# Kernel optimization log

Measured on AMD Instinct MI355X. Metric: run time of the kernel, lower is better.

## Reference

```python
import jax, jax.numpy as jnp
import numpy as np

B, T, NIN = 128, 256, 16
H1 = H2 = 512
NACT = 4
SLOPE = 25.0  # snntorch FastSigmoid default slope

@jax.custom_vjp
def spike(x):
    return (x > 0).astype(x.dtype)

def _spike_fwd(x):
    return (x > 0).astype(x.dtype), x

def _spike_bwd(x, g):
    # FastSigmoid surrogate: d/dx = 1 / (slope*|x| + 1)^2
    return (g / (SLOPE * jnp.abs(x) + 1.0) ** 2,)

spike.defvjp(_spike_fwd, _spike_bwd)

def setup_inputs() -> dict:
    key = jax.random.key(0)
    ks = jax.random.split(key, 12)
    def lin(k, fan_in, shape):
        lim = 1.0 / np.sqrt(fan_in)
        return jax.random.uniform(k, shape, jnp.float32, -lim, lim)
    return {
        "batch": jax.random.uniform(ks[0], (B, T, NIN), jnp.float32, 0.0, 2.5),
        "W1": lin(ks[1], NIN, (H1, NIN)), "b1": lin(ks[2], NIN, (H1,)),
        "beta1": jax.random.uniform(ks[3], (H1,), jnp.float32),
        "thr1": jax.random.uniform(ks[4], (H1,), jnp.float32),
        "W2": lin(ks[5], H1, (H2, H1)), "b2": lin(ks[6], H1, (H2,)),
        "beta2": jax.random.uniform(ks[7], (H2,), jnp.float32),
        "thr2": jax.random.uniform(ks[8], (H2,), jnp.float32),
        "Wa": lin(ks[9], H2, (NACT, H2)), "ba": lin(ks[10], H2, (NACT,)),
        "beta_act": jnp.float32(0.95),
        "inp_min": jnp.float32(0.0),
        "inp_max": jnp.float32(2.5),
    }

def _lif_subtract(cur, mem, beta, thr):
    # snntorch Leaky: reset from PRE-update membrane, detached; subtract reset
    reset = jax.lax.stop_gradient((mem - thr > 0).astype(mem.dtype))
    mem = jnp.clip(beta, 0.0, 1.0) * mem + cur - reset * thr
    return spike(mem - thr), mem

def reference(batch, W1, b1, beta1, thr1, W2, b2, beta2, thr2, Wa, ba, beta_act, inp_min, inp_max):
    Bb = batch.shape[0]
    x_seq = jnp.swapaxes(batch, 0, 1)  # [T, B, NIN]
    mem1 = jnp.zeros((Bb, W1.shape[0]), batch.dtype)
    mem2 = jnp.zeros((Bb, W2.shape[0]), batch.dtype)
    mem_a = jnp.zeros((Bb, Wa.shape[0]), batch.dtype)

    def step(carry, x):
        mem1, mem2, mem_a = carry
        x = (x - inp_min) / (inp_max - inp_min)
        spk1, mem1 = _lif_subtract(x @ W1.T + b1, mem1, beta1, thr1)
        spk2, mem2 = _lif_subtract(spk1 @ W2.T + b2, mem2, beta2, thr2)
        act = spk2 @ Wa.T + ba
        # action_lif: reset_mechanism='none', beta=0.95 learnable
        mem_a = jnp.clip(beta_act, 0.0, 1.0) * mem_a + act
        return (mem1, mem2, mem_a), mem_a.reshape(-1)  # torch: mem_act.reshape((1,-1))

    _, vals = jax.lax.scan(step, (mem1, mem2, mem_a), x_seq)
    # torch.stack(values, dim=1) of (1, B*NACT) tensors -> (1, T, B*NACT)
    return vals[None, :, :]
```

## Files before the change

### kernel.cpp

```cpp
#include <hip/hip_runtime.h>
#include <stdint.h>

typedef __attribute__((ext_vector_type(8))) short short8;
typedef __attribute__((ext_vector_type(4))) float f32x4;

#define T_STEPS 256
#define BATCH   128

#define LDS_BARRIER() asm volatile("s_waitcnt lgkmcnt(0)\n\ts_barrier" ::: "memory")

static __device__ inline unsigned short f2bf(float f) {
    unsigned int u = __float_as_uint(f);
    unsigned int r = u + 0x7FFFu + ((u >> 16) & 1u);
    return (unsigned short)(r >> 16);
}
static __device__ inline unsigned pack_hi16(unsigned a, unsigned b) {
    return (a >> 16) | (b & 0xFFFF0000u);
}

__global__ __launch_bounds__(256) void k_prep(
    const float* __restrict__ W2, const float* __restrict__ W1,
    const float* __restrict__ b1, const float* __restrict__ thr1,
    const float* __restrict__ imin_p, const float* __restrict__ imax_p,
    const float* __restrict__ batch,
    unsigned short* __restrict__ W2hi, unsigned short* __restrict__ W2lo,
    unsigned short* __restrict__ W1rows, float* __restrict__ b1s,
    unsigned short* __restrict__ Xf)
{
    int blk = blockIdx.x, tid = threadIdx.x;
    if (blk < 256) {
        int gid = blk * 256 + tid;
        f32x4 wv = *(const f32x4*)(W2 + (size_t)gid * 4);
        unsigned short hi[4], lo[4];
#pragma unroll
        for (int e = 0; e < 4; ++e) {
            float wf = wv[e];
            unsigned short h = f2bf(wf);
            float hf = __uint_as_float(((unsigned int)h) << 16);
            hi[e] = h;
            lo[e] = f2bf(wf - hf);
        }
        uint2 ph, pl;
        ph.x = (unsigned)hi[0] | ((unsigned)hi[1] << 16);
        ph.y = (unsigned)hi[2] | ((unsigned)hi[3] << 16);
        pl.x = (unsigned)lo[0] | ((unsigned)lo[1] << 16);
        pl.y = (unsigned)lo[2] | ((unsigned)lo[3] << 16);
        *(uint2*)(W2hi + (size_t)gid * 4) = ph;
        *(uint2*)(W2lo + (size_t)gid * 4) = pl;
    } else if (blk < 258) {
        int h = (blk - 256) * 256 + tid;
        float wsc = 1.0f / thr1[h];
        unsigned short row[64];
#pragma unroll
        for (int k = 0; k < 16; ++k) {
            float wv = W1[h * 16 + k] * wsc;
            unsigned a = __float_as_uint(wv) & 0xFFFF0000u;
            float r1 = wv - __uint_as_float(a);
            unsigned m = __float_as_uint(r1) & 0xFFFF0000u;
            float r2 = r1 - __uint_as_float(m);
            unsigned l = __float_as_uint(r2) & 0xFFFF0000u;
            row[k]      = (unsigned short)(a >> 16);
            row[16 + k] = (unsigned short)(m >> 16);
            row[32 + k] = (unsigned short)(l >> 16);
            row[48 + k] = 0;
        }
        b1s[h] = b1[h] * wsc;
        uint4* dst = (uint4*)(W1rows + (size_t)h * 64);
#pragma unroll
        for (int i = 0; i < 8; ++i) dst[i] = ((uint4*)row)[i];
    } else {
        int gid   = (blk - 258) * 256 + tid;
        int lane  = gid & 63;
        int btile = (gid >> 6) & 7;
        int t     = gid >> 9;
        int q     = lane >> 4, m15 = lane & 15;
        int b     = btile * 16 + m15;
        float imin = imin_p[0];
        float isc  = 1.0f / (imax_p[0] - imin);
        const float* xp = batch + ((size_t)b * T_STEPS + t) * 16 + (q & 1) * 8;
        unsigned uh[8], um[8], ul[8];
#pragma unroll
        for (int j = 0; j < 8; ++j) {
            float xv = (xp[j] - imin) * isc;
            unsigned a = __float_as_uint(xv) & 0xFFFF0000u;
            float r1 = xv - __uint_as_float(a);
            unsigned m = __float_as_uint(r1) & 0xFFFF0000u;
            float r2 = r1 - __uint_as_float(m);
            unsigned l = __float_as_uint(r2) & 0xFFFF0000u;
            uh[j] = a; um[j] = m; ul[j] = l;
        }
        uint4 B1, B2, XL;
        B1.x = pack_hi16(uh[0], uh[1]); B1.y = pack_hi16(uh[2], uh[3]);
        B1.z = pack_hi16(uh[4], uh[5]); B1.w = pack_hi16(uh[6], uh[7]);
        B2.x = pack_hi16(um[0], um[1]); B2.y = pack_hi16(um[2], um[3]);
        B2.z = pack_hi16(um[4], um[5]); B2.w = pack_hi16(um[6], um[7]);
        XL.x = pack_hi16(ul[0], ul[1]); XL.y = pack_hi16(ul[2], ul[3]);
        XL.z = pack_hi16(ul[4], ul[5]); XL.w = pack_hi16(ul[6], ul[7]);
        uint4 B3 = (q < 2) ? XL : B1;
        uint4 B4 = (q < 2) ? XL : B2;
        unsigned short* dst = Xf + (((size_t)t * 8 + btile) * 4) * 512 + lane * 8;
        *(uint4*)(dst +    0) = B1;
        *(uint4*)(dst +  512) = B2;
        *(uint4*)(dst + 1024) = B3;
        *(uint4*)(dst + 1536) = B4;
    }
}

__global__ __launch_bounds__(1024, 4) void k_main(
    const unsigned short* __restrict__ Xf,
    const unsigned short* __restrict__ W2hi, const unsigned short* __restrict__ W2lo,
    const unsigned short* __restrict__ W1rows, const float* __restrict__ b1s,
    const float* __restrict__ beta1, const float* __restrict__ b2,
    const float* __restrict__ beta2, const float* __restrict__ thr2,
    unsigned short* __restrict__ spkbits)
{
    __shared__ unsigned short Aw[8192];
    __shared__ float Cbuf[2][4096];

    int tid  = threadIdx.x;
    int lane = tid & 63;
    int w    = tid >> 6;
    int q    = lane >> 4, m15 = lane & 15;
    int btile = blockIdx.x & 7;
    int slice = blockIdx.x >> 3;

    short8 A1[2], A2[2], A3[2];
#pragma unroll
    for (int c = 0; c < 2; ++c) {
        const unsigned short* rp = W1rows + (size_t)(w * 32 + c * 16 + m15) * 64;
        A1[c] = *(const short8*)(rp + q * 8);
        A2[c] = *(const short8*)(rp + q * 8 + (q >> 1) * 16);
        A3[c] = *(const short8*)(rp + 16 + q * 8);
    }
    int jg = slice * 16 + m15;
    short8 bhi = *(const short8*)(W2hi + (size_t)jg * 512 + w * 32 + q * 8);
    short8 blo = *(const short8*)(W2lo + (size_t)jg * 512 + w * 32 + q * 8);

    f32x4 b14[2], bet1[2];
#pragma unroll
    for (int c = 0; c < 2; ++c) {
        int h0 = w * 32 + c * 16 + q * 4;
        b14[c] = *(const f32x4*)(b1s + h0);
        f32x4 bb = *(const f32x4*)(beta1 + h0);
#pragma unroll
        for (int r = 0; r < 4; ++r) bet1[c][r] = fminf(fmaxf(bb[r], 0.0f), 1.0f);
    }
    float m1[8], spk1f[8];
#pragma unroll
    for (int i = 0; i < 8; ++i) { m1[i] = 0.0f; spk1f[i] = 0.0f; }

    float beta2r = fminf(fmaxf(beta2[jg], 0.0f), 1.0f);
    float thr2r  = thr2[jg];
    float nthr2  = -thr2r;
    float b2r    = b2[jg];
    float m2 = 0.0f, spk2f = 0.0f;

    const unsigned short* xbase = Xf + ((size_t)btile * 4) * 512 + lane * 8;
    uint4 xc[4], xn[4];
#pragma unroll
    for (int f = 0; f < 4; ++f) xc[f] = *(const uint4*)(xbase + f * 512);

    unsigned short* myAw = Aw + w * 512;
    int wr0 = (0 * 2 + (q >> 1)) * 128 + (m15 ^ (q >> 1)) * 8 + (q & 1) * 4;
    int wr1 = (1 * 2 + (q >> 1)) * 128 + (m15 ^ (q >> 1)) * 8 + (q & 1) * 4;
    int rdo = (q * 16 + (m15 ^ (q & 1))) * 8;

    auto body = [&](int ts, uint4* xcur, uint4* xnx) __attribute__((always_inline)) {
        int buf = ts & 1;
        int tn = (ts + 1 < T_STEPS) ? ts + 1 : ts;
        const unsigned short* xp = xbase + (size_t)tn * 16384;
#pragma unroll
        for (int f = 0; f < 4; ++f) xnx[f] = *(const uint4*)(xp + f * 512);

        union { uint4 u; short8 s; } Bf[4];
#pragma unroll
        for (int f = 0; f < 4; ++f) Bf[f].u = xcur[f];
        f32x4 D[2];
#pragma unroll
        for (int c = 0; c < 2; ++c) {
            D[c] = b14[c];
            D[c] = __builtin_amdgcn_mfma_f32_16x16x32_bf16(A1[c], Bf[0].s, D[c], 0, 0, 0);
            D[c] = __builtin_amdgcn_mfma_f32_16x16x32_bf16(A1[c], Bf[1].s, D[c], 0, 0, 0);
            D[c] = __builtin_amdgcn_mfma_f32_16x16x32_bf16(A2[c], Bf[2].s, D[c], 0, 0, 0);
            D[c] = __builtin_amdgcn_mfma_f32_16x16x32_bf16(A3[c], Bf[3].s, D[c], 0, 0, 0);
        }
#pragma unroll
        for (int i = 0; i < 8; ++i) {
            int c = i >> 2, r = i & 3;
            float mv = fmaf(bet1[c][r], m1[i], D[c][r]);
            mv -= spk1f[i];
            bool sp = mv > 1.0f;
            m1[i] = mv;
            spk1f[i] = sp ? 1.0f : 0.0f;
        }
        {
            uint2 pk0, pk1;
            pk0.x = pack_hi16(__float_as_uint(spk1f[0]), __float_as_uint(spk1f[1]));
            pk0.y = pack_hi16(__float_as_uint(spk1f[2]), __float_as_uint(spk1f[3]));
            pk1.x = pack_hi16(__float_as_uint(spk1f[4]), __float_as_uint(spk1f[5]));
            pk1.y = pack_hi16(__float_as_uint(spk1f[6]), __float_as_uint(spk1f[7]));
            *(uint2*)(myAw + wr0) = pk0;
            *(uint2*)(myAw + wr1) = pk1;
        }
        union { uint4 u; short8 s; } af;
        af.u = *(uint4*)(myAw + rdo);
        f32x4 C2 = { 0.f, 0.f, 0.f, 0.f };
        C2 = __builtin_amdgcn_mfma_f32_16x16x32_bf16(af.s, bhi, C2, 0, 0, 0);
        C2 = __builtin_amdgcn_mfma_f32_16x16x32_bf16(af.s, blo, C2, 0, 0, 0);
#pragma unroll
        for (int r = 0; r < 4; ++r)
            Cbuf[buf][r * 1024 + w * 64 + lane] = C2[r];
        LDS_BARRIER();
        if (w < 4) {
            float cur2 = b2r;
#pragma unroll
            for (int wp = 0; wp < 16; ++wp) cur2 += Cbuf[buf][w * 1024 + wp * 64 + lane];
            m2 = fmaf(beta2r, m2, cur2);
            m2 = fmaf(spk2f, nthr2, m2);
            bool sp2 = m2 > thr2r;
            spk2f = sp2 ? 1.0f : 0.0f;
            unsigned long long mask = __ballot(sp2);
            if (lane < 4) {
                unsigned short v = (unsigned short)(mask >> (lane * 16));
                spkbits[((size_t)ts * BATCH + btile * 16 + lane * 4 + w) * 32 + slice] = v;
            }
        }
    };

#pragma unroll 1
    for (int ts = 0; ts < T_STEPS; ts += 2) {
        body(ts, xc, xn);
        body(ts + 1, xn, xc);
    }
}

__global__ __launch_bounds__(256) void k_act(
    const unsigned short* __restrict__ spkbits,
    const float* __restrict__ Wa, const float* __restrict__ ba,
    const float* __restrict__ beta_act_p, float* __restrict__ out)
{
    __shared__ f32x4 waT[512];
    __shared__ f32x4 sc[256];
    int tid = threadIdx.x;
    int b   = blockIdx.x;

    for (int j = tid; j < 512; j += 256) {
        f32x4 v = { Wa[j], Wa[512 + j], Wa[1024 + j], Wa[1536 + j] };
        waT[j] = v;
    }
    float bact = fminf(fmaxf(beta_act_p[0], 0.0f), 1.0f);
    f32x4 acc = { ba[0], ba[1], ba[2], ba[3] };
    __syncthreads();

    const unsigned short* sp = spkbits + ((size_t)tid * BATCH + b) * 32;
    unsigned int wbuf[16];
#pragma unroll
    for (int r = 0; r < 4; ++r) {
        uint4 v = *(const uint4*)(sp + r * 8);
        wbuf[r*4+0] = v.x; wbuf[r*4+1] = v.y; wbuf[r*4+2] = v.z; wbuf[r*4+3] = v.w;
    }
    for (int s = 0; s < 32; ++s) {
        unsigned int wd = (wbuf[s >> 1] >> ((s & 1) * 16)) & 0xFFFFu;
#pragma unroll
        for (int i = 0; i < 16; ++i) {
            float sel = ((wd >> i) & 1u) ? 1.0f : 0.0f;
            f32x4 wv = waT[s * 16 + i];
            acc[0] = fmaf(sel, wv[0], acc[0]);
            acc[1] = fmaf(sel, wv[1], acc[1]);
            acc[2] = fmaf(sel, wv[2], acc[2]);
            acc[3] = fmaf(sel, wv[3], acc[3]);
        }
    }
    sc[tid] = acc;
    __syncthreads();
    float bd = bact;
    for (int d = 1; d < 256; d <<= 1) {
        f32x4 cv = sc[tid];
        f32x4 pv = { 0.f, 0.f, 0.f, 0.f };
        if (tid >= d) pv = sc[tid - d];
        __syncthreads();
        cv[0] = fmaf(bd, pv[0], cv[0]);
        cv[1] = fmaf(bd, pv[1], cv[1]);
        cv[2] = fmaf(bd, pv[2], cv[2]);
        cv[3] = fmaf(bd, pv[3], cv[3]);
        sc[tid] = cv;
        __syncthreads();
        bd *= bd;
    }
    f32x4 res = sc[tid];
    *(f32x4*)(out + (size_t)tid * 512 + b * 4) = res;
}

extern "C" void kernel_launch(void* const* d_in, const int* in_sizes, int n_in,
                              void* d_out, int out_size, void* d_ws, size_t ws_size,
                              hipStream_t stream)
{
    const float* batch    = (const float*)d_in[0];
    const float* W1       = (const float*)d_in[1];
    const float* b1       = (const float*)d_in[2];
    const float* beta1    = (const float*)d_in[3];
    const float* thr1     = (const float*)d_in[4];
    const float* W2       = (const float*)d_in[5];
    const float* b2       = (const float*)d_in[6];
    const float* beta2    = (const float*)d_in[7];
    const float* thr2     = (const float*)d_in[8];
    const float* Wa       = (const float*)d_in[9];
    const float* ba       = (const float*)d_in[10];
    const float* beta_act = (const float*)d_in[11];
    const float* inp_min  = (const float*)d_in[12];
    const float* inp_max  = (const float*)d_in[13];
    float* out            = (float*)d_out;

    char* ws = (char*)d_ws;
    unsigned short* W2hi    = (unsigned short*)ws;
    unsigned short* W2lo    = (unsigned short*)(ws + (512u << 10));
    unsigned short* W1rows  = (unsigned short*)(ws + (1u << 20));
    float*          b1s     = (float*)(ws + (1u << 20) + (64u << 10));
    unsigned short* Xf      = (unsigned short*)(ws + (2u << 20));
    unsigned short* spkbits = (unsigned short*)(ws + (10u << 20));

    hipLaunchKernelGGL(k_prep, dim3(770), dim3(256), 0, stream,
                       W2, W1, b1, thr1, inp_min, inp_max, batch,
                       W2hi, W2lo, W1rows, b1s, Xf);
    hipLaunchKernelGGL(k_main, dim3(256), dim3(1024), 0, stream,
                       Xf, W2hi, W2lo, W1rows, b1s, beta1, b2, beta2, thr2, spkbits);
    hipLaunchKernelGGL(k_act, dim3(128), dim3(256), 0, stream, spkbits, Wa, ba, beta_act, out);
}
```

Baseline: 308.7 us.

## Drop redundant x fragment MFMA and spread layer-2 reduction across all waves

The layer-1 input projection now uses three split-bf16 fragments instead of four. This removes one MFMA per tile and one global load stream per step, and shrinks the staged input buffer. The cross-wave reduction of layer-2 partial sums is re-laid out with a padded transposed LDS buffer. All 16 waves now each sum four partials and finish with shuffles, where before four waves serially summed sixteen. The change removes work from the per-step critical path, but it relies on the dropped fragment being redundant for accuracy.

```diff
diff --git a/kernel.cpp b/kernel.cpp
--- a/kernel.cpp
+++ b/kernel.cpp
@@ -97,12 +97,10 @@
         XL.x = pack_hi16(ul[0], ul[1]); XL.y = pack_hi16(ul[2], ul[3]);
         XL.z = pack_hi16(ul[4], ul[5]); XL.w = pack_hi16(ul[6], ul[7]);
         uint4 B3 = (q < 2) ? XL : B1;
-        uint4 B4 = (q < 2) ? XL : B2;
-        unsigned short* dst = Xf + (((size_t)t * 8 + btile) * 4) * 512 + lane * 8;
+        unsigned short* dst = Xf + (((size_t)t * 8 + btile) * 3) * 512 + lane * 8;
         *(uint4*)(dst +    0) = B1;
         *(uint4*)(dst +  512) = B2;
         *(uint4*)(dst + 1024) = B3;
-        *(uint4*)(dst + 1536) = B4;
     }
 }
 
@@ -115,7 +113,7 @@
     unsigned short* __restrict__ spkbits)
 {
     __shared__ unsigned short Aw[8192];
-    __shared__ float Cbuf[2][4096];
+    __shared__ float Cbuf[2][4352];
 
     int tid  = threadIdx.x;
     int lane = tid & 63;
@@ -124,13 +122,12 @@
     int btile = blockIdx.x & 7;
     int slice = blockIdx.x >> 3;
 
-    short8 A1[2], A2[2], A3[2];
+    short8 A1[2], A2[2];
 #pragma unroll
     for (int c = 0; c < 2; ++c) {
         const unsigned short* rp = W1rows + (size_t)(w * 32 + c * 16 + m15) * 64;
         A1[c] = *(const short8*)(rp + q * 8);
         A2[c] = *(const short8*)(rp + q * 8 + (q >> 1) * 16);
-        A3[c] = *(const short8*)(rp + 16 + q * 8);
     }
     int jg = slice * 16 + m15;
     short8 bhi = *(const short8*)(W2hi + (size_t)jg * 512 + w * 32 + q * 8);
@@ -155,26 +152,27 @@
     float b2r    = b2[jg];
     float m2 = 0.0f, spk2f = 0.0f;
 
-    const unsigned short* xbase = Xf + ((size_t)btile * 4) * 512 + lane * 8;
-    uint4 xc[4], xn[4];
-#pragma unroll
-    for (int f = 0; f < 4; ++f) xc[f] = *(const uint4*)(xbase + f * 512);
+    const unsigned short* xbase = Xf + ((size_t)btile * 3) * 512 + lane * 8;
+    uint4 xc[3], xn[3];
+#pragma unroll
+    for (int f = 0; f < 3; ++f) xc[f] = *(const uint4*)(xbase + f * 512);
 
     unsigned short* myAw = Aw + w * 512;
     int wr0 = (0 * 2 + (q >> 1)) * 128 + (m15 ^ (q >> 1)) * 8 + (q & 1) * 4;
     int wr1 = (1 * 2 + (q >> 1)) * 128 + (m15 ^ (q >> 1)) * 8 + (q & 1) * 4;
     int rdo = (q * 16 + (m15 ^ (q & 1))) * 8;
+    int p4  = (lane >> 4) * 4;
 
     auto body = [&](int ts, uint4* xcur, uint4* xnx) __attribute__((always_inline)) {
         int buf = ts & 1;
         int tn = (ts + 1 < T_STEPS) ? ts + 1 : ts;
-        const unsigned short* xp = xbase + (size_t)tn * 16384;
-#pragma unroll
-        for (int f = 0; f < 4; ++f) xnx[f] = *(const uint4*)(xp + f * 512);
-
-        union { uint4 u; short8 s; } Bf[4];
-#pragma unroll
-        for (int f = 0; f < 4; ++f) Bf[f].u = xcur[f];
+        const unsigned short* xp = xbase + (size_t)tn * 12288;
+#pragma unroll
+        for (int f = 0; f < 3; ++f) xnx[f] = *(const uint4*)(xp + f * 512);
+
+        union { uint4 u; short8 s; } Bf[3];
+#pragma unroll
+        for (int f = 0; f < 3; ++f) Bf[f].u = xcur[f];
         f32x4 D[2];
 #pragma unroll
         for (int c = 0; c < 2; ++c) {
@@ -182,7 +180,6 @@
             D[c] = __builtin_amdgcn_mfma_f32_16x16x32_bf16(A1[c], Bf[0].s, D[c], 0, 0, 0);
             D[c] = __builtin_amdgcn_mfma_f32_16x16x32_bf16(A1[c], Bf[1].s, D[c], 0, 0, 0);
             D[c] = __builtin_amdgcn_mfma_f32_16x16x32_bf16(A2[c], Bf[2].s, D[c], 0, 0, 0);
-            D[c] = __builtin_amdgcn_mfma_f32_16x16x32_bf16(A3[c], Bf[3].s, D[c], 0, 0, 0);
         }
 #pragma unroll
         for (int i = 0; i < 8; ++i) {
@@ -209,20 +206,27 @@
         C2 = __builtin_amdgcn_mfma_f32_16x16x32_bf16(af.s, blo, C2, 0, 0, 0);
 #pragma unroll
         for (int r = 0; r < 4; ++r)
-            Cbuf[buf][r * 1024 + w * 64 + lane] = C2[r];
+            Cbuf[buf][(q * 4 + r) * 272 + m15 * 17 + w] = C2[r];
         LDS_BARRIER();
-        if (w < 4) {
-            float cur2 = b2r;
-#pragma unroll
-            for (int wp = 0; wp < 16; ++wp) cur2 += Cbuf[buf][w * 1024 + wp * 64 + lane];
+        {
+            float s0, s1, s2, s3;
+            int base = w * 272 + m15 * 17 + p4;
+            s0 = Cbuf[buf][base + 0];
+            s1 = Cbuf[buf][base + 1];
+            s2 = Cbuf[buf][base + 2];
+            s3 = Cbuf[buf][base + 3];
+            float s = (s0 + s1) + (s2 + s3);
+            s += __shfl_xor(s, 16, 64);
+            s += __shfl_xor(s, 32, 64);
+            float cur2 = b2r + s;
             m2 = fmaf(beta2r, m2, cur2);
             m2 = fmaf(spk2f, nthr2, m2);
             bool sp2 = m2 > thr2r;
             spk2f = sp2 ? 1.0f : 0.0f;
             unsigned long long mask = __ballot(sp2);
-            if (lane < 4) {
-                unsigned short v = (unsigned short)(mask >> (lane * 16));
-                spkbits[((size_t)ts * BATCH + btile * 16 + lane * 4 + w) * 32 + slice] = v;
+            if (lane == 0) {
+                spkbits[((size_t)ts * BATCH + btile * 16 + w) * 32 + slice] =
+                    (unsigned short)(mask & 0xFFFFu);
             }
         }
     };
@@ -317,7 +321,7 @@
     unsigned short* W1rows  = (unsigned short*)(ws + (1u << 20));
     float*          b1s     = (float*)(ws + (1u << 20) + (64u << 10));
     unsigned short* Xf      = (unsigned short*)(ws + (2u << 20));
-    unsigned short* spkbits = (unsigned short*)(ws + (10u << 20));
+    unsigned short* spkbits = (unsigned short*)(ws + (8u << 20));
 
     hipLaunchKernelGGL(k_prep, dim3(770), dim3(256), 0, stream,
                        W2, W1, b1, thr1, inp_min, inp_max, batch,
```

Result: no change. 313.4 us (+1.5%).
